# Kernel tuning notes

Measured on AMD Instinct MI355X. Metric: run time of the kernel, lower is better.

## Reference

```python
import jax, jax.numpy as jnp
import numpy as np

# powers used in the generalized loss (self.range_p); static int constants
RANGE_P = (1, 2)


def setup_inputs() -> dict:
    key = jax.random.key(0)
    k1, k2, k3 = jax.random.split(key, 3)
    n, L, P = 8192, 96, len(RANGE_P)
    y_true = jax.random.normal(k1, (n, L), dtype=jnp.float32)
    y_pred = jax.random.normal(k2, (n, L), dtype=jnp.float32)
    weights = jax.random.uniform(k3, (P, L, L), dtype=jnp.float32)
    return {"y_true": y_true, "y_pred": y_pred, "weights": weights}


def _abs_diff(y_true, y_pred):
    """Vectorized build of the (n, L, L) abs_diff tensor.

    Column j=0:  |y_true - y_pred|  at every position i.
    Column j>=1: rows i in [0, L-j): |(yt[i]-yt[i+j]) - (yp[i]-yp[i+j])|
                 = |e[i] - e[i+j]| with e = y_true - y_pred; zeros elsewhere.
    """
    n, L = y_true.shape
    e = y_true - y_pred                      # (n, L)
    i = jnp.arange(L)[:, None]               # row index (L, 1)
    j = jnp.arange(L)[None, :]               # lag index  (1, L)
    k = i + j                                # partner index (L, L)
    valid = k < L
    kc = jnp.minimum(k, L - 1)               # clipped gather index
    pair = jnp.abs(e[:, :, None] - e[:, kc])  # (n, L, L): |e_i - e_{i+j}|
    D = jnp.where(j == 0,
                  jnp.abs(e)[:, :, None],     # lag-0 column is |e_i|
                  jnp.where(valid, pair, 0.0))
    return D


def reference(y_true, y_pred, weights):
    n, L = y_true.shape
    D = _abs_diff(y_true, y_pred)            # (n, L, L)
    loss = jnp.float32(0.0)
    for p_idx, p in enumerate(RANGE_P):
        # weights[p_idx] is (L, L); broadcasts over the example axis
        loss = loss + jnp.sum(jnp.power(D, p) * weights[p_idx])
    return loss / (L * n)
```

## Files before the change

### kernel.cpp

```cpp
#include <hip/hip_runtime.h>

#define LL 96
#define NT 256
#define BROWS 32
#define KPT 12
#define YBLK 3

__global__ __launch_bounds__(NT) void gl_loss_main(
    const float* __restrict__ yt, const float* __restrict__ yp,
    const float* __restrict__ w, float* __restrict__ out,
    int n, float inv_scale) {
  __shared__ __align__(16) float e_lds[BROWS][LL];

  const int t  = threadIdx.x;
  const int c  = blockIdx.y * NT + t;
  const int i  = c >> 3;
  const int kc = c & 7;
  const int k0 = kc * KPT;

  float w0r[KPT], w1r[KPT];
#pragma unroll
  for (int jj = 0; jj < KPT; ++jj) {
    int k = k0 + jj;
    bool valid = (k > i);
    w0r[jj] = valid ? w[i * LL + (k - i)] : 0.f;
    w1r[jj] = valid ? w[LL * LL + i * LL + (k - i)] : 0.f;
  }
  const bool dg = (i >= k0) && (i < k0 + KPT);
  const float w0d = dg ? w[i * LL] : 0.f;
  const float w1d = dg ? w[LL * LL + i * LL] : 0.f;

  const int b0 = blockIdx.x * BROWS;
  float4* ef = (float4*)&e_lds[0][0];
  for (int f = t; f < BROWS * LL / 4; f += NT) {
    int row = f / (LL / 4);
    int c4  = f - row * (LL / 4);
    int b = b0 + row;
    float4 v = make_float4(0.f, 0.f, 0.f, 0.f);
    if (b < n) {
      const float4 a = *(const float4*)&yt[b * LL + c4 * 4];
      const float4 p = *(const float4*)&yp[b * LL + c4 * 4];
      v = make_float4(a.x - p.x, a.y - p.y, a.z - p.z, a.w - p.w);
    }
    ef[f] = v;
  }
  __syncthreads();

  float acc0 = 0.f, acc1 = 0.f;
#pragma unroll 2
  for (int b = 0; b < BROWS; ++b) {
    float ei = e_lds[b][i];
    float4 vA = *(const float4*)&e_lds[b][k0];
    float4 vB = *(const float4*)&e_lds[b][k0 + 4];
    float4 vC = *(const float4*)&e_lds[b][k0 + 8];
    float ek[KPT] = {vA.x, vA.y, vA.z, vA.w, vB.x, vB.y, vB.z, vB.w,
                     vC.x, vC.y, vC.z, vC.w};
#pragma unroll
    for (int jj = 0; jj < KPT; ++jj) {
      float d = fabsf(ei - ek[jj]);
      if (jj & 1)
        acc1 = fmaf(d, fmaf(d, w1r[jj], w0r[jj]), acc1);
      else
        acc0 = fmaf(d, fmaf(d, w1r[jj], w0r[jj]), acc0);
    }
    float a = fabsf(ei);
    acc1 = fmaf(a, fmaf(a, w1d, w0d), acc1);
  }
  float acc = acc0 + acc1;

#pragma unroll
  for (int off = 32; off; off >>= 1) acc += __shfl_down(acc, off);
  __shared__ float wsum[NT / 64];
  if ((t & 63) == 0) wsum[t >> 6] = acc;
  __syncthreads();
  if (t == 0) {
    float s = wsum[0] + wsum[1] + wsum[2] + wsum[3];
    atomicAdd(out, s * inv_scale);
  }
}

extern "C" void kernel_launch(void* const* d_in, const int* in_sizes, int n_in,
                              void* d_out, int out_size, void* d_ws, size_t ws_size,
                              hipStream_t stream) {
  const float* yt = (const float*)d_in[0];
  const float* yp = (const float*)d_in[1];
  const float* w  = (const float*)d_in[2];
  float* out = (float*)d_out;
  int n = in_sizes[0] / LL;

  dim3 grid((n + BROWS - 1) / BROWS, YBLK);
  gl_loss_main<<<grid, NT, 0, stream>>>(yt, yp, w, out, n,
                                        1.0f / (float(LL) * float(n)));
}
```

Measured before the change: 75.98 us.

## Fold the three i-slices into each thread to reuse loaded e rows

Each thread now handles three row indices i (ig, ig+32, ig+64) instead of one, and the grid drops its y dimension. Rows of e are loaded into LDS once per block rather than three times across y-blocks, and each set of ek values read from LDS is reused across three i values. BROWS is halved to keep the grid large. This triples the weight registers per thread (72 plus 6), which raises register pressure and may lower occupancy.

```diff
diff --git a/kernel.cpp b/kernel.cpp
--- a/kernel.cpp
+++ b/kernel.cpp
@@ -2,9 +2,9 @@
 
 #define LL 96
 #define NT 256
-#define BROWS 32
+#define BROWS 16
 #define KPT 12
-#define YBLK 3
+#define NI 3
 
 __global__ __launch_bounds__(NT) void gl_loss_main(
     const float* __restrict__ yt, const float* __restrict__ yp,
@@ -13,58 +13,66 @@
   __shared__ __align__(16) float e_lds[BROWS][LL];
 
   const int t  = threadIdx.x;
-  const int c  = blockIdx.y * NT + t;
-  const int i  = c >> 3;
-  const int kc = c & 7;
+  const int ig = t >> 3;
+  const int kc = t & 7;
   const int k0 = kc * KPT;
 
-  float w0r[KPT], w1r[KPT];
+  float w0r[NI][KPT], w1r[NI][KPT], w0d[NI], w1d[NI];
 #pragma unroll
-  for (int jj = 0; jj < KPT; ++jj) {
-    int k = k0 + jj;
-    bool valid = (k > i);
-    w0r[jj] = valid ? w[i * LL + (k - i)] : 0.f;
-    w1r[jj] = valid ? w[LL * LL + i * LL + (k - i)] : 0.f;
+  for (int m = 0; m < NI; ++m) {
+    int i = ig + 32 * m;
+#pragma unroll
+    for (int jj = 0; jj < KPT; ++jj) {
+      int k = k0 + jj;
+      bool valid = (k > i);
+      w0r[m][jj] = valid ? w[i * LL + (k - i)] : 0.f;
+      w1r[m][jj] = valid ? w[LL * LL + i * LL + (k - i)] : 0.f;
+    }
+    bool dg = (i >= k0) && (i < k0 + KPT);
+    w0d[m] = dg ? w[i * LL] : 0.f;
+    w1d[m] = dg ? w[LL * LL + i * LL] : 0.f;
   }
-  const bool dg = (i >= k0) && (i < k0 + KPT);
-  const float w0d = dg ? w[i * LL] : 0.f;
-  const float w1d = dg ? w[LL * LL + i * LL] : 0.f;
 
   const int b0 = blockIdx.x * BROWS;
-  float4* ef = (float4*)&e_lds[0][0];
-  for (int f = t; f < BROWS * LL / 4; f += NT) {
-    int row = f / (LL / 4);
-    int c4  = f - row * (LL / 4);
-    int b = b0 + row;
-    float4 v = make_float4(0.f, 0.f, 0.f, 0.f);
-    if (b < n) {
-      const float4 a = *(const float4*)&yt[b * LL + c4 * 4];
-      const float4 p = *(const float4*)&yp[b * LL + c4 * 4];
-      v = make_float4(a.x - p.x, a.y - p.y, a.z - p.z, a.w - p.w);
+  {
+    float4* ef = (float4*)&e_lds[0][0];
+    for (int f = t; f < BROWS * LL / 4; f += NT) {
+      int row = f / (LL / 4);
+      int c4  = f - row * (LL / 4);
+      int b = b0 + row;
+      float4 v = make_float4(0.f, 0.f, 0.f, 0.f);
+      if (b < n) {
+        const float4 a = *(const float4*)&yt[b * LL + c4 * 4];
+        const float4 p = *(const float4*)&yp[b * LL + c4 * 4];
+        v = make_float4(a.x - p.x, a.y - p.y, a.z - p.z, a.w - p.w);
+      }
+      ef[f] = v;
     }
-    ef[f] = v;
   }
   __syncthreads();
 
   float acc0 = 0.f, acc1 = 0.f;
 #pragma unroll 2
   for (int b = 0; b < BROWS; ++b) {
-    float ei = e_lds[b][i];
     float4 vA = *(const float4*)&e_lds[b][k0];
     float4 vB = *(const float4*)&e_lds[b][k0 + 4];
     float4 vC = *(const float4*)&e_lds[b][k0 + 8];
     float ek[KPT] = {vA.x, vA.y, vA.z, vA.w, vB.x, vB.y, vB.z, vB.w,
                      vC.x, vC.y, vC.z, vC.w};
 #pragma unroll
-    for (int jj = 0; jj < KPT; ++jj) {
-      float d = fabsf(ei - ek[jj]);
-      if (jj & 1)
-        acc1 = fmaf(d, fmaf(d, w1r[jj], w0r[jj]), acc1);
-      else
-        acc0 = fmaf(d, fmaf(d, w1r[jj], w0r[jj]), acc0);
+    for (int m = 0; m < NI; ++m) {
+      float ei = e_lds[b][ig + 32 * m];
+#pragma unroll
+      for (int jj = 0; jj < KPT; ++jj) {
+        float d = fabsf(ei - ek[jj]);
+        if (jj & 1)
+          acc1 = fmaf(d, fmaf(d, w1r[m][jj], w0r[m][jj]), acc1);
+        else
+          acc0 = fmaf(d, fmaf(d, w1r[m][jj], w0r[m][jj]), acc0);
+      }
+      float a = fabsf(ei);
+      acc1 = fmaf(a, fmaf(a, w1d[m], w0d[m]), acc1);
     }
-    float a = fabsf(ei);
-    acc1 = fmaf(a, fmaf(a, w1d, w0d), acc1);
   }
   float acc = acc0 + acc1;
 
@@ -88,7 +96,7 @@
   float* out = (float*)d_out;
   int n = in_sizes[0] / LL;
 
-  dim3 grid((n + BROWS - 1) / BROWS, YBLK);
+  dim3 grid((n + BROWS - 1) / BROWS, 1);
   gl_loss_main<<<grid, NT, 0, stream>>>(yt, yp, w, out, n,
                                         1.0f / (float(LL) * float(n)));
 }
```

After: 73.93 us. 2.7% less time.
